# Kernel optimization log

Hardware: AMD Instinct MI355X
Metric: run time of the kernel (lower is better)

Reference implementation:

```python
import jax, jax.numpy as jnp
import numpy as np

N = 10000      # nodes
E = 320000     # edges (before self-loops)
D_IN = 256
HID = 128
HEADS = 4
D_OUT = 256
SLOPE = 0.2    # PyG GATConv default negative_slope


def setup_inputs() -> dict:
    key = jax.random.key(0)
    ks = jax.random.split(key, 10)
    s = 0.05
    return {
        "x": jax.random.normal(ks[0], (N, D_IN), dtype=jnp.float32),
        "edge_index": jax.random.randint(ks[1], (2, E), 0, N),
        # layer 1: in=256 -> heads=4, out=128, concat
        "W1": jax.random.normal(ks[2], (D_IN, HEADS * HID), dtype=jnp.float32) * s,
        "a1_src": jax.random.normal(ks[3], (HEADS, HID), dtype=jnp.float32) * s,
        "a1_dst": jax.random.normal(ks[4], (HEADS, HID), dtype=jnp.float32) * s,
        "b1": jax.random.normal(ks[5], (HEADS * HID,), dtype=jnp.float32) * s,
        # layer 2: in=512 -> heads=1, out=256, no concat
        "W2": jax.random.normal(ks[6], (HEADS * HID, D_OUT), dtype=jnp.float32) * s,
        "a2_src": jax.random.normal(ks[7], (1, D_OUT), dtype=jnp.float32) * s,
        "a2_dst": jax.random.normal(ks[8], (1, D_OUT), dtype=jnp.float32) * s,
        "b2": jax.random.normal(ks[9], (D_OUT,), dtype=jnp.float32) * s,
    }


def gat_conv(x, src, dst, W, a_src, a_dst, bias, heads, out_dim, concat):
    """PyG-style GATConv (eval mode, self-loops pre-added to src/dst)."""
    n = x.shape[0]
    h = (x @ W).reshape(n, heads, out_dim)            # [N, H, F]
    # per-edge attention logits: LeakyReLU(a_src.h_src + a_dst.h_dst)
    as_n = (h * a_src).sum(-1)                         # [N, H]
    ad_n = (h * a_dst).sum(-1)                         # [N, H]
    logit = jax.nn.leaky_relu(as_n[src] + ad_n[dst], negative_slope=SLOPE)  # [E, H]
    # segment softmax over edges grouped by destination node
    logit = logit - jax.ops.segment_max(logit, dst, num_segments=n)[dst]
    ex = jnp.exp(logit)
    alpha = ex / jax.ops.segment_sum(ex, dst, num_segments=n)[dst]          # [E, H]
    # weighted scatter-aggregation of source messages
    out = jax.ops.segment_sum(h[src] * alpha[:, :, None], dst, num_segments=n)  # [N, H, F]
    out = out.reshape(n, heads * out_dim) if concat else out.mean(axis=1)
    return out + bias


def reference(x, edge_index, W1, a1_src, a1_dst, b1, W2, a2_src, a2_dst, b2):
    # add self-loops once (PyG GATConv default add_self_loops=True)
    loops = jnp.arange(N, dtype=edge_index.dtype)
    src = jnp.concatenate([edge_index[0], loops])
    dst = jnp.concatenate([edge_index[1], loops])
    h = gat_conv(x, src, dst, W1, a1_src, a1_dst, b1, HEADS, HID, True)
    h = jax.nn.elu(h)  # dropout is identity at eval
    return gat_conv(h, src, dst, W2, a2_src, a2_dst, b2, 1, D_OUT, False)
```

## Files before the change

kernel.cpp:

```cpp
#include <hip/hip_runtime.h>

#define N_NODES 10000
#define E_RAW   320000
#define E_TOT   330000
#define D_IN    256
#define HID     128
#define HEADS   4
#define F1      512
#define D_OUT   256
#define SLOPE   0.2f

typedef __attribute__((ext_vector_type(8))) short bf16x8;
typedef __attribute__((ext_vector_type(4))) float f32x4;

__device__ __forceinline__ float bf2f(ushort u) {
    return __uint_as_float(((uint)u) << 16);
}
__device__ __forceinline__ ushort f2bf(float x) {
    uint u = __float_as_uint(x);
    uint r = (u + 0x7FFFu + ((u >> 16) & 1u)) >> 16;
    return (ushort)r;
}
__device__ __forceinline__ float bfu_lo(uint u) { return __uint_as_float(u << 16); }
__device__ __forceinline__ float bfu_hi(uint u) { return __uint_as_float(u & 0xFFFF0000u); }


__global__ __launch_bounds__(256) void k_hist(const int* __restrict__ ei, int* __restrict__ deg) {
    int e = blockIdx.x * 256 + threadIdx.x;
    if (e < E_TOT) {
        int dst = (e < E_RAW) ? ei[E_RAW + e] : (e - E_RAW);
        atomicAdd(&deg[dst], 1);
    }
}

#define SCAN_CHUNK 40

__global__ __launch_bounds__(256) void k_scan(const int* __restrict__ deg,
                                              int* __restrict__ row_start,
                                              int* __restrict__ cursor) {
    __shared__ int tots[256];
    int tid = threadIdx.x;
    int base = tid * SCAN_CHUNK;
    int loc[SCAN_CHUNK];
    int s = 0;
    #pragma unroll
    for (int k = 0; k < SCAN_CHUNK; k++) {
        int idx = base + k;
        int v = (idx < N_NODES) ? deg[idx] : 0;
        loc[k] = s;
        s += v;
    }
    tots[tid] = s;
    __syncthreads();
    for (int off = 1; off < 256; off <<= 1) {
        int t = (tid >= off) ? tots[tid - off] : 0;
        __syncthreads();
        tots[tid] += t;
        __syncthreads();
    }
    int excl = tots[tid] - s;
    #pragma unroll
    for (int k = 0; k < SCAN_CHUNK; k++) {
        int idx = base + k;
        if (idx < N_NODES) {
            int r = excl + loc[k];
            row_start[idx] = r;
            cursor[idx]    = r;
        }
    }
    if (tid == 255) row_start[N_NODES] = E_TOT;
}

__global__ __launch_bounds__(256) void k_scatter(const int* __restrict__ ei,
                                                 int* __restrict__ cursor,
                                                 int* __restrict__ csr_src) {
    int e = blockIdx.x * 256 + threadIdx.x;
    if (e < E_TOT) {
        int src = (e < E_RAW) ? ei[e] : (e - E_RAW);
        int dst = (e < E_RAW) ? ei[E_RAW + e] : (e - E_RAW);
        int pos = atomicAdd(&cursor[dst], 1);
        csr_src[pos] = src;
    }
}


__global__ __launch_bounds__(256) void k_castT(const float* __restrict__ in,
                                               ushort* __restrict__ outp,
                                               int K, int N) {
    int i = blockIdx.x * 256 + threadIdx.x;
    if (i < K * N) {
        int k = i / N, n = i - k * N;
        outp[(size_t)n * K + k] = f2bf(in[i]);
    }
}


template<bool A_F32>
__global__ __launch_bounds__(256) void k_gemm_mfma(const void* __restrict__ Av,
                                                   const ushort* __restrict__ Bh,
                                                   ushort* __restrict__ C,
                                                   int M, int N, int K) {
    __shared__ ushort sA[128][72];
    __shared__ ushort sB[64][72];

    const int tid = threadIdx.x;
    const int lane = tid & 63;
    const int wid = tid >> 6;
    const int wr = wid >> 1;
    const int wc = wid & 1;
    const int m0 = blockIdx.y * 128;
    const int n0 = blockIdx.x * 64;
    const int fr = lane & 15;
    const int fk = (lane >> 4) * 8;

    f32x4 acc[4][2];
    #pragma unroll
    for (int i = 0; i < 4; i++)
        #pragma unroll
        for (int j = 0; j < 2; j++) acc[i][j] = (f32x4){0.f, 0.f, 0.f, 0.f};

    for (int k0 = 0; k0 < K; k0 += 64) {
        if (A_F32) {
            const float* A = (const float*)Av;
            #pragma unroll
            for (int t = 0; t < 8; t++) {
                int c = tid + 256 * t;
                int row = c >> 4, kc = (c & 15) << 2;
                int gr = m0 + row;
                gr = gr < M ? gr : M - 1;
                float4 av = *(const float4*)&A[(size_t)gr * K + k0 + kc];
                ushort4 u;
                u.x = f2bf(av.x); u.y = f2bf(av.y); u.z = f2bf(av.z); u.w = f2bf(av.w);
                *(ushort4*)&sA[row][kc] = u;
            }
        } else {
            const ushort* A = (const ushort*)Av;
            #pragma unroll
            for (int t = 0; t < 4; t++) {
                int c = tid + 256 * t;
                int row = c >> 3, kc = (c & 7) << 3;
                int gr = m0 + row;
                gr = gr < M ? gr : M - 1;
                *(float4*)&sA[row][kc] = *(const float4*)&A[(size_t)gr * K + k0 + kc];
            }
        }
        #pragma unroll
        for (int t = 0; t < 2; t++) {
            int c = tid + 256 * t;
            int col = c >> 3, kc = (c & 7) << 3;
            size_t go = (size_t)(n0 + col) * K + k0 + kc;
            *(float4*)&sB[col][kc] = *(const float4*)&Bh[go];
        }
        __syncthreads();
        #pragma unroll
        for (int kk = 0; kk < 2; kk++) {
            int kb = kk * 32 + fk;
            bf16x8 a_f[4], b_f[2];
            #pragma unroll
            for (int i = 0; i < 4; i++)
                a_f[i] = *(const bf16x8*)&sA[wr * 64 + i * 16 + fr][kb];
            #pragma unroll
            for (int j = 0; j < 2; j++)
                b_f[j] = *(const bf16x8*)&sB[wc * 32 + j * 16 + fr][kb];
            #pragma unroll
            for (int i = 0; i < 4; i++)
                #pragma unroll
                for (int j = 0; j < 2; j++)
                    acc[i][j] = __builtin_amdgcn_mfma_f32_16x16x32_bf16(a_f[i], b_f[j], acc[i][j], 0, 0, 0);
        }
        __syncthreads();
    }

    #pragma unroll
    for (int i = 0; i < 4; i++) {
        #pragma unroll
        for (int j = 0; j < 2; j++) {
            int row_base = m0 + wr * 64 + i * 16 + ((lane >> 4) << 2);
            int col = n0 + wc * 32 + j * 16 + (lane & 15);
            #pragma unroll
            for (int q = 0; q < 4; q++) {
                int r = row_base + q;
                if (r < M) C[(size_t)r * N + col] = f2bf(acc[i][j][q]);
            }
        }
    }
}


__global__ __launch_bounds__(256) void k_attn_vec1(const ushort* __restrict__ h1,
                                                   const float* __restrict__ a1s,
                                                   const float* __restrict__ a1d,
                                                   float* __restrict__ as1,
                                                   float* __restrict__ ad1) {
    int node = blockIdx.x;
    int tid = threadIdx.x;
    int wave = tid >> 6;
    int lane = tid & 63;
    const ushort* hr = h1 + (size_t)node * F1 + wave * HID;
    const float* svp = a1s + wave * HID;
    const float* dvp = a1d + wave * HID;
    float h0 = bf2f(hr[lane]), h1v = bf2f(hr[lane + 64]);
    float s_ = h0 * svp[lane] + h1v * svp[lane + 64];
    float d_ = h0 * dvp[lane] + h1v * dvp[lane + 64];
    #pragma unroll
    for (int off = 32; off >= 1; off >>= 1) {
        s_ += __shfl_xor(s_, off, 64);
        d_ += __shfl_xor(d_, off, 64);
    }
    if (lane == 0) {
        as1[node * 4 + wave] = s_;
        ad1[node * 4 + wave] = d_;
    }
}

__global__ __launch_bounds__(256) void k_attn_vec2(const ushort* __restrict__ h2,
                                                   const float* __restrict__ a2s,
                                                   const float* __restrict__ a2d,
                                                   float* __restrict__ as2,
                                                   float* __restrict__ ad2) {
    int node = blockIdx.x * 4 + (threadIdx.x >> 6);
    int lane = threadIdx.x & 63;
    uint2 hv = *(const uint2*)(h2 + (size_t)node * D_OUT + lane * 4);
    float h0 = bfu_lo(hv.x), h1v = bfu_hi(hv.x), h2v = bfu_lo(hv.y), h3 = bfu_hi(hv.y);
    float4 sv = *(const float4*)(a2s + lane * 4);
    float4 dv = *(const float4*)(a2d + lane * 4);
    float s_ = h0 * sv.x + h1v * sv.y + h2v * sv.z + h3 * sv.w;
    float d_ = h0 * dv.x + h1v * dv.y + h2v * dv.z + h3 * dv.w;
    #pragma unroll
    for (int off = 32; off >= 1; off >>= 1) {
        s_ += __shfl_xor(s_, off, 64);
        d_ += __shfl_xor(d_, off, 64);
    }
    if (lane == 0) { as2[node] = s_; ad2[node] = d_; }
}


__device__ __forceinline__ void fma8(uint4 v, float e, float* acc) {
    acc[0] += bfu_lo(v.x) * e; acc[1] += bfu_hi(v.x) * e;
    acc[2] += bfu_lo(v.y) * e; acc[3] += bfu_hi(v.y) * e;
    acc[4] += bfu_lo(v.z) * e; acc[5] += bfu_hi(v.z) * e;
    acc[6] += bfu_lo(v.w) * e; acc[7] += bfu_hi(v.w) * e;
}

__global__ __launch_bounds__(256) void k_edge1(const int* __restrict__ row_start,
                                               const int* __restrict__ csr_src,
                                               const ushort* __restrict__ h1,
                                               const float* __restrict__ as1,
                                               const float* __restrict__ ad1,
                                               const float* __restrict__ b1,
                                               ushort* __restrict__ heluh) {
    int node = blockIdx.x * 4 + (threadIdx.x >> 6);
    int lane = threadIdx.x & 63;
    int start = row_start[node];
    int end   = row_start[node + 1];
    int h_lane = lane >> 4;

    float adl = ad1[node * 4 + h_lane];

    float acc[8] = {0,0,0,0,0,0,0,0};
    float sum = 0.f;
    const size_t lo8 = (size_t)lane * 8;

    int i = start;
    for (; i + 8 <= end; i += 8) {
        int s[8];
        #pragma unroll
        for (int k = 0; k < 8; k++) s[k] = csr_src[i + k];
        float l[8];
        #pragma unroll
        for (int k = 0; k < 8; k++) l[k] = as1[s[k] * 4 + h_lane];
        uint4 v[8];
        #pragma unroll
        for (int k = 0; k < 8; k++) v[k] = *(const uint4*)(h1 + (size_t)s[k] * F1 + lo8);
        #pragma unroll
        for (int k = 0; k < 8; k++) {
            float t = l[k] + adl;
            t = t > 0.f ? t : SLOPE * t;
            float e = __expf(t);
            sum += e;
            fma8(v[k], e, acc);
        }
    }
    for (; i < end; i++) {
        int s0 = csr_src[i];
        float t = as1[s0 * 4 + h_lane] + adl;
        uint4 v0 = *(const uint4*)(h1 + (size_t)s0 * F1 + lo8);
        t = t > 0.f ? t : SLOPE * t;
        float e = __expf(t);
        sum += e;
        fma8(v0, e, acc);
    }
    float inv = 1.f / sum;

    size_t o = (size_t)node * F1 + lo8;
    const float* bp = b1 + lo8;
    uint pk[4];
    #pragma unroll
    for (int j = 0; j < 4; j++) {
        float v0 = acc[2*j]   * inv + bp[2*j];
        float v1 = acc[2*j+1] * inv + bp[2*j+1];
        v0 = v0 > 0.f ? v0 : (__expf(v0) - 1.f);
        v1 = v1 > 0.f ? v1 : (__expf(v1) - 1.f);
        pk[j] = (uint)f2bf(v0) | ((uint)f2bf(v1) << 16);
    }
    *(uint4*)&heluh[o] = make_uint4(pk[0], pk[1], pk[2], pk[3]);
}

__global__ __launch_bounds__(256) void k_edge2(const int* __restrict__ row_start,
                                               const int* __restrict__ csr_src,
                                               const ushort* __restrict__ h2,
                                               const float* __restrict__ as2,
                                               const float* __restrict__ ad2,
                                               const float* __restrict__ b2,
                                               float* __restrict__ out) {
    int node = blockIdx.x * 4 + (threadIdx.x >> 6);
    int lane = threadIdx.x & 63;
    int start = row_start[node];
    int end   = row_start[node + 1];

    float ad = ad2[node];

    float acc[4] = {0,0,0,0};
    float sum = 0.f;
    const size_t lo4 = (size_t)lane * 4;

    int i = start;
    for (; i + 8 <= end; i += 8) {
        int s[8];
        #pragma unroll
        for (int k = 0; k < 8; k++) s[k] = csr_src[i + k];
        float l[8];
        #pragma unroll
        for (int k = 0; k < 8; k++) l[k] = as2[s[k]];
        uint2 v[8];
        #pragma unroll
        for (int k = 0; k < 8; k++) v[k] = *(const uint2*)(h2 + (size_t)s[k] * D_OUT + lo4);
        #pragma unroll
        for (int k = 0; k < 8; k++) {
            float t = l[k] + ad;
            t = t > 0.f ? t : SLOPE * t;
            float e = __expf(t);
            sum += e;
            acc[0] += bfu_lo(v[k].x) * e; acc[1] += bfu_hi(v[k].x) * e;
            acc[2] += bfu_lo(v[k].y) * e; acc[3] += bfu_hi(v[k].y) * e;
        }
    }
    for (; i < end; i++) {
        int s0 = csr_src[i];
        float t = as2[s0] + ad;
        uint2 v0 = *(const uint2*)(h2 + (size_t)s0 * D_OUT + lo4);
        t = t > 0.f ? t : SLOPE * t;
        float e = __expf(t);
        sum += e;
        acc[0] += bfu_lo(v0.x) * e; acc[1] += bfu_hi(v0.x) * e;
        acc[2] += bfu_lo(v0.y) * e; acc[3] += bfu_hi(v0.y) * e;
    }
    float inv = 1.f / sum;
    float4 r;
    r.x = acc[0] * inv + b2[lo4 + 0];
    r.y = acc[1] * inv + b2[lo4 + 1];
    r.z = acc[2] * inv + b2[lo4 + 2];
    r.w = acc[3] * inv + b2[lo4 + 3];
    *(float4*)&out[(size_t)node * D_OUT + lo4] = r;
}


extern "C" void kernel_launch(void* const* d_in, const int* in_sizes, int n_in,
                              void* d_out, int out_size, void* d_ws, size_t ws_size,
                              hipStream_t stream) {
    const float* x   = (const float*)d_in[0];
    const int*   ei  = (const int*)d_in[1];
    const float* W1  = (const float*)d_in[2];
    const float* a1s = (const float*)d_in[3];
    const float* a1d = (const float*)d_in[4];
    const float* b1  = (const float*)d_in[5];
    const float* W2  = (const float*)d_in[6];
    const float* a2s = (const float*)d_in[7];
    const float* a2d = (const float*)d_in[8];
    const float* b2  = (const float*)d_in[9];
    float* out = (float*)d_out;

    char* ws = (char*)d_ws;
    size_t off = 0;
    auto take = [&](size_t bytes) {
        char* p = ws + off;
        off += (bytes + 255) & ~(size_t)255;
        return p;
    };
    int*    deg       = (int*)take(sizeof(int) * N_NODES);
    int*    row_start = (int*)take(sizeof(int) * (N_NODES + 1));
    int*    cursor    = (int*)take(sizeof(int) * N_NODES);
    int*    csr_src   = (int*)take(sizeof(int) * E_TOT);
    ushort* w1h       = (ushort*)take(sizeof(ushort) * D_IN * F1);
    ushort* w2h       = (ushort*)take(sizeof(ushort) * F1 * D_OUT);
    ushort* h1        = (ushort*)take(sizeof(ushort) * (size_t)N_NODES * F1);
    float*  as1       = (float*)take(sizeof(float) * N_NODES * 4);
    float*  ad1       = (float*)take(sizeof(float) * N_NODES * 4);
    ushort* heluh     = (ushort*)take(sizeof(ushort) * (size_t)N_NODES * F1);
    ushort* h2        = (ushort*)take(sizeof(ushort) * (size_t)N_NODES * D_OUT);
    float*  as2       = (float*)take(sizeof(float) * N_NODES);
    float*  ad2       = (float*)take(sizeof(float) * N_NODES);

    hipMemsetAsync(deg, 0, sizeof(int) * N_NODES, stream);

    int eblocks = (E_TOT + 255) / 256;
    k_hist<<<eblocks, 256, 0, stream>>>(ei, deg);
    k_scan<<<1, 256, 0, stream>>>(deg, row_start, cursor);
    k_scatter<<<eblocks, 256, 0, stream>>>(ei, cursor, csr_src);

    k_castT<<<(D_IN * F1 + 255) / 256, 256, 0, stream>>>(W1, w1h, D_IN, F1);
    k_castT<<<(F1 * D_OUT + 255) / 256, 256, 0, stream>>>(W2, w2h, F1, D_OUT);

    k_gemm_mfma<true><<<dim3(F1 / 64, (N_NODES + 127) / 128), 256, 0, stream>>>(
        (const void*)x, w1h, h1, N_NODES, F1, D_IN);
    k_attn_vec1<<<N_NODES, 256, 0, stream>>>(h1, a1s, a1d, as1, ad1);
    k_edge1<<<N_NODES / 4, 256, 0, stream>>>(row_start, csr_src, h1, as1, ad1, b1, heluh);

    k_gemm_mfma<false><<<dim3(D_OUT / 64, (N_NODES + 127) / 128), 256, 0, stream>>>(
        (const void*)heluh, w2h, h2, N_NODES, D_OUT, F1);
    k_attn_vec2<<<N_NODES / 4, 256, 0, stream>>>(h2, a2s, a2d, as2, ad2);
    k_edge2<<<N_NODES / 4, 256, 0, stream>>>(row_start, csr_src, h2, as2, ad2, b2, out);
}
```

Baseline: 175.3 us.

## Use direct global-to-LDS loads with XOR swizzle in GEMM, pre-cast x to bf16

The GEMM now stages A and B tiles with global_load_lds (16-byte direct-to-LDS loads) into an unpadded, XOR-swizzled shared layout, replacing register-staged copies and the padded arrays. Converting x to bf16 moves into a separate vectorized cast kernel so a single bf16 GEMM path serves both layers. The layer-1 attention-vector kernel now handles four nodes per block with 8-wide loads, and the memset becomes a small zero kernel. The cost is an extra pass over x and an extra bf16 buffer, in exchange for cheaper tile loading in the GEMM.

```diff
diff --git a/kernel.cpp b/kernel.cpp
--- a/kernel.cpp
+++ b/kernel.cpp
@@ -24,6 +24,17 @@
 __device__ __forceinline__ float bfu_lo(uint u) { return __uint_as_float(u << 16); }
 __device__ __forceinline__ float bfu_hi(uint u) { return __uint_as_float(u & 0xFFFF0000u); }
 
+__device__ __forceinline__ void gload_lds16(const void* g, void* l) {
+    __builtin_amdgcn_global_load_lds(
+        (const __attribute__((address_space(1))) void*)g,
+        (__attribute__((address_space(3))) void*)l, 16, 0, 0);
+}
+
+
+__global__ __launch_bounds__(256) void k_zero(int* __restrict__ p, int n) {
+    int i = blockIdx.x * 256 + threadIdx.x;
+    if (i < n) p[i] = 0;
+}
 
 __global__ __launch_bounds__(256) void k_hist(const int* __restrict__ ei, int* __restrict__ deg) {
     int e = blockIdx.x * 256 + threadIdx.x;
@@ -84,6 +95,21 @@
 }
 
 
+__global__ __launch_bounds__(256) void k_cast8(const float* __restrict__ in,
+                                               ushort* __restrict__ outp, int n8) {
+    int i = blockIdx.x * 256 + threadIdx.x;
+    if (i < n8) {
+        float4 a = *(const float4*)&in[(size_t)i * 8];
+        float4 b = *(const float4*)&in[(size_t)i * 8 + 4];
+        uint4 u;
+        u.x = (uint)f2bf(a.x) | ((uint)f2bf(a.y) << 16);
+        u.y = (uint)f2bf(a.z) | ((uint)f2bf(a.w) << 16);
+        u.z = (uint)f2bf(b.x) | ((uint)f2bf(b.y) << 16);
+        u.w = (uint)f2bf(b.z) | ((uint)f2bf(b.w) << 16);
+        *(uint4*)&outp[(size_t)i * 8] = u;
+    }
+}
+
 __global__ __launch_bounds__(256) void k_castT(const float* __restrict__ in,
                                                ushort* __restrict__ outp,
                                                int K, int N) {
@@ -95,13 +121,12 @@
 }
 
 
-template<bool A_F32>
-__global__ __launch_bounds__(256) void k_gemm_mfma(const void* __restrict__ Av,
-                                                   const ushort* __restrict__ Bh,
-                                                   ushort* __restrict__ C,
-                                                   int M, int N, int K) {
-    __shared__ ushort sA[128][72];
-    __shared__ ushort sB[64][72];
+__global__ __launch_bounds__(256) void k_gemm(const ushort* __restrict__ A,
+                                              const ushort* __restrict__ B,
+                                              ushort* __restrict__ C,
+                                              int M, int N, int K) {
+    __shared__ ushort sA[128 * 64];
+    __shared__ ushort sB[64 * 64];
 
     const int tid = threadIdx.x;
     const int lane = tid & 63;
@@ -111,7 +136,10 @@
     const int m0 = blockIdx.y * 128;
     const int n0 = blockIdx.x * 64;
     const int fr = lane & 15;
-    const int fk = (lane >> 4) * 8;
+    const int fs = lane >> 4;
+
+    const int rowc = lane >> 3;
+    const int slot = (lane & 7) ^ rowc;
 
     f32x4 acc[4][2];
     #pragma unroll
@@ -120,48 +148,34 @@
         for (int j = 0; j < 2; j++) acc[i][j] = (f32x4){0.f, 0.f, 0.f, 0.f};
 
     for (int k0 = 0; k0 < K; k0 += 64) {
-        if (A_F32) {
-            const float* A = (const float*)Av;
-            #pragma unroll
-            for (int t = 0; t < 8; t++) {
-                int c = tid + 256 * t;
-                int row = c >> 4, kc = (c & 15) << 2;
-                int gr = m0 + row;
-                gr = gr < M ? gr : M - 1;
-                float4 av = *(const float4*)&A[(size_t)gr * K + k0 + kc];
-                ushort4 u;
-                u.x = f2bf(av.x); u.y = f2bf(av.y); u.z = f2bf(av.z); u.w = f2bf(av.w);
-                *(ushort4*)&sA[row][kc] = u;
-            }
-        } else {
-            const ushort* A = (const ushort*)Av;
-            #pragma unroll
-            for (int t = 0; t < 4; t++) {
-                int c = tid + 256 * t;
-                int row = c >> 3, kc = (c & 7) << 3;
-                int gr = m0 + row;
-                gr = gr < M ? gr : M - 1;
-                *(float4*)&sA[row][kc] = *(const float4*)&A[(size_t)gr * K + k0 + kc];
-            }
+        #pragma unroll
+        for (int t = 0; t < 4; t++) {
+            int c = wid + 4 * t;
+            int gr = m0 + c * 8 + rowc;
+            gr = gr < M ? gr : M - 1;
+            gload_lds16(A + (size_t)gr * K + k0 + slot * 8, &sA[c * 512]);
         }
         #pragma unroll
         for (int t = 0; t < 2; t++) {
-            int c = tid + 256 * t;
-            int col = c >> 3, kc = (c & 7) << 3;
-            size_t go = (size_t)(n0 + col) * K + k0 + kc;
-            *(float4*)&sB[col][kc] = *(const float4*)&Bh[go];
+            int c = wid + 4 * t;
+            int gc = n0 + c * 8 + rowc;
+            gload_lds16(B + (size_t)gc * K + k0 + slot * 8, &sB[c * 512]);
         }
         __syncthreads();
         #pragma unroll
         for (int kk = 0; kk < 2; kk++) {
-            int kb = kk * 32 + fk;
+            int sbase = kk * 4 + fs;
             bf16x8 a_f[4], b_f[2];
             #pragma unroll
-            for (int i = 0; i < 4; i++)
-                a_f[i] = *(const bf16x8*)&sA[wr * 64 + i * 16 + fr][kb];
+            for (int i = 0; i < 4; i++) {
+                int r = wr * 64 + i * 16 + fr;
+                a_f[i] = *(const bf16x8*)&sA[r * 64 + ((sbase ^ (r & 7)) << 3)];
+            }
             #pragma unroll
-            for (int j = 0; j < 2; j++)
-                b_f[j] = *(const bf16x8*)&sB[wc * 32 + j * 16 + fr][kb];
+            for (int j = 0; j < 2; j++) {
+                int cc = wc * 32 + j * 16 + fr;
+                b_f[j] = *(const bf16x8*)&sB[cc * 64 + ((sbase ^ (cc & 7)) << 3)];
+            }
             #pragma unroll
             for (int i = 0; i < 4; i++)
                 #pragma unroll
@@ -192,24 +206,26 @@
                                                    const float* __restrict__ a1d,
                                                    float* __restrict__ as1,
                                                    float* __restrict__ ad1) {
-    int node = blockIdx.x;
-    int tid = threadIdx.x;
-    int wave = tid >> 6;
-    int lane = tid & 63;
-    const ushort* hr = h1 + (size_t)node * F1 + wave * HID;
-    const float* svp = a1s + wave * HID;
-    const float* dvp = a1d + wave * HID;
-    float h0 = bf2f(hr[lane]), h1v = bf2f(hr[lane + 64]);
-    float s_ = h0 * svp[lane] + h1v * svp[lane + 64];
-    float d_ = h0 * dvp[lane] + h1v * dvp[lane + 64];
-    #pragma unroll
-    for (int off = 32; off >= 1; off >>= 1) {
+    int node = blockIdx.x * 4 + (threadIdx.x >> 6);
+    int lane = threadIdx.x & 63;
+    uint4 hv = *(const uint4*)(h1 + (size_t)node * F1 + (size_t)lane * 8);
+    const float* sp = a1s + lane * 8;
+    const float* dp = a1d + lane * 8;
+    float4 sa = *(const float4*)sp, sb = *(const float4*)(sp + 4);
+    float4 da = *(const float4*)dp, db = *(const float4*)(dp + 4);
+    float h0 = bfu_lo(hv.x), h1v = bfu_hi(hv.x), h2v = bfu_lo(hv.y), h3 = bfu_hi(hv.y);
+    float h4 = bfu_lo(hv.z), h5 = bfu_hi(hv.z), h6 = bfu_lo(hv.w), h7 = bfu_hi(hv.w);
+    float s_ = h0*sa.x + h1v*sa.y + h2v*sa.z + h3*sa.w + h4*sb.x + h5*sb.y + h6*sb.z + h7*sb.w;
+    float d_ = h0*da.x + h1v*da.y + h2v*da.z + h3*da.w + h4*db.x + h5*db.y + h6*db.z + h7*db.w;
+    #pragma unroll
+    for (int off = 8; off >= 1; off >>= 1) {
         s_ += __shfl_xor(s_, off, 64);
         d_ += __shfl_xor(d_, off, 64);
     }
-    if (lane == 0) {
-        as1[node * 4 + wave] = s_;
-        ad1[node * 4 + wave] = d_;
+    if ((lane & 15) == 0) {
+        int head = lane >> 4;
+        as1[node * 4 + head] = s_;
+        ad1[node * 4 + head] = d_;
     }
 }
 
@@ -391,6 +407,7 @@
     int*    row_start = (int*)take(sizeof(int) * (N_NODES + 1));
     int*    cursor    = (int*)take(sizeof(int) * N_NODES);
     int*    csr_src   = (int*)take(sizeof(int) * E_TOT);
+    ushort* xb        = (ushort*)take(sizeof(ushort) * (size_t)N_NODES * D_IN);
     ushort* w1h       = (ushort*)take(sizeof(ushort) * D_IN * F1);
     ushort* w2h       = (ushort*)take(sizeof(ushort) * F1 * D_OUT);
     ushort* h1        = (ushort*)take(sizeof(ushort) * (size_t)N_NODES * F1);
@@ -401,23 +418,21 @@
     float*  as2       = (float*)take(sizeof(float) * N_NODES);
     float*  ad2       = (float*)take(sizeof(float) * N_NODES);
 
-    hipMemsetAsync(deg, 0, sizeof(int) * N_NODES, stream);
-
     int eblocks = (E_TOT + 255) / 256;
+    k_zero<<<(N_NODES + 255) / 256, 256, 0, stream>>>(deg, N_NODES);
     k_hist<<<eblocks, 256, 0, stream>>>(ei, deg);
     k_scan<<<1, 256, 0, stream>>>(deg, row_start, cursor);
     k_scatter<<<eblocks, 256, 0, stream>>>(ei, cursor, csr_src);
 
+    k_cast8<<<(N_NODES * D_IN / 8 + 255) / 256, 256, 0, stream>>>(x, xb, N_NODES * D_IN / 8);
     k_castT<<<(D_IN * F1 + 255) / 256, 256, 0, stream>>>(W1, w1h, D_IN, F1);
     k_castT<<<(F1 * D_OUT + 255) / 256, 256, 0, stream>>>(W2, w2h, F1, D_OUT);
 
-    k_gemm_mfma<true><<<dim3(F1 / 64, (N_NODES + 127) / 128), 256, 0, stream>>>(
-        (const void*)x, w1h, h1, N_NODES, F1, D_IN);
-    k_attn_vec1<<<N_NODES, 256, 0, stream>>>(h1, a1s, a1d, as1, ad1);
+    k_gemm<<<dim3(F1 / 64, (N_NODES + 127) / 128), 256, 0, stream>>>(xb, w1h, h1, N_NODES, F1, D_IN);
+    k_attn_vec1<<<N_NODES / 4, 256, 0, stream>>>(h1, a1s, a1d, as1, ad1);
     k_edge1<<<N_NODES / 4, 256, 0, stream>>>(row_start, csr_src, h1, as1, ad1, b1, heluh);
 
-    k_gemm_mfma<false><<<dim3(D_OUT / 64, (N_NODES + 127) / 128), 256, 0, stream>>>(
-        (const void*)heluh, w2h, h2, N_NODES, D_OUT, F1);
+    k_gemm<<<dim3(D_OUT / 64, (N_NODES + 127) / 128), 256, 0, stream>>>(heluh, w2h, h2, N_NODES, D_OUT, F1);
     k_attn_vec2<<<N_NODES / 4, 256, 0, stream>>>(h2, a2s, a2d, as2, ad2);
     k_edge2<<<N_NODES / 4, 256, 0, stream>>>(row_start, csr_src, h2, as2, ad2, b2, out);
 }
```

After: 168.1 us. 4.1% less time.
